# Kernel tuning notes

Measured on AMD Instinct MI355X. Metric: run time of the kernel, lower is better.

Reference implementation:

```python
import jax, jax.numpy as jnp
import numpy as np

EMBED_DIM = 768
N_HEADS = 12
HEAD_DIM = EMBED_DIM // N_HEADS
B, S = 8, 1024


def setup_inputs() -> dict:
    key = jax.random.key(0)
    ks = jax.random.split(key, 7)
    sc = 1.0 / np.sqrt(HEAD_DIM)
    return {
        "sequences": jax.random.normal(ks[0], (B, S, EMBED_DIM), dtype=jnp.float32),
        # per-head Linear weights stored [H, in, out] (torch Linear is x @ W.T + b;
        # with random init the layout convention is equivalent math)
        "Wq": jax.random.normal(ks[1], (N_HEADS, HEAD_DIM, HEAD_DIM), dtype=jnp.float32) * sc,
        "bq": jax.random.normal(ks[2], (N_HEADS, HEAD_DIM), dtype=jnp.float32) * 0.01,
        "Wk": jax.random.normal(ks[3], (N_HEADS, HEAD_DIM, HEAD_DIM), dtype=jnp.float32) * sc,
        "bk": jax.random.normal(ks[4], (N_HEADS, HEAD_DIM), dtype=jnp.float32) * 0.01,
        "Wv": jax.random.normal(ks[5], (N_HEADS, HEAD_DIM, HEAD_DIM), dtype=jnp.float32) * sc,
        "bv": jax.random.normal(ks[6], (N_HEADS, HEAD_DIM), dtype=jnp.float32) * 0.01,
    }


def reference(sequences, Wq, bq, Wk, bk, Wv, bv):
    b, s, d = sequences.shape
    h, hd = Wq.shape[0], Wq.shape[1]
    x = sequences.reshape(b, s, h, hd)              # split embed dim into heads
    q = jnp.einsum("bshd,hde->bshe", x, Wq) + bq    # per-head linear (block-diag GEMM)
    k = jnp.einsum("bshd,hde->bshe", x, Wk) + bk
    v = jnp.einsum("bshd,hde->bshe", x, Wv) + bv
    # NOTE: original module applies NO 1/sqrt(head_dim) scaling
    logits = jnp.einsum("bshe,bthe->bhst", q, k)    # [B,H,S,S]
    attn = jax.nn.softmax(logits, axis=-1)
    out = jnp.einsum("bhst,bthe->bshe", attn, v)    # [B,S,H,hd]
    return out.reshape(b, s, d)
```

## Files before the change

kernel.cpp:

```cpp
#include <hip/hip_runtime.h>
#include <stdint.h>

#define EMBED 768
#define NH 12
#define HD 64
#define Bsz 8
#define Ssz 1024
#define LOG2E 1.44269504088896f

typedef __attribute__((ext_vector_type(4))) float f32x4;
typedef __attribute__((ext_vector_type(8))) _Float16 f16x8;
typedef __attribute__((ext_vector_type(4))) _Float16 f16x4;

__launch_bounds__(256)
__global__ void qkv_proj(const float* __restrict__ x,
                         const float* __restrict__ Wq, const float* __restrict__ bq,
                         const float* __restrict__ Wk, const float* __restrict__ bk,
                         const float* __restrict__ Wv, const float* __restrict__ bv,
                         _Float16* __restrict__ Qb, _Float16* __restrict__ Kb,
                         _Float16* __restrict__ Vt)
{
    __shared__ _Float16 Xs[128 * 72];
    __shared__ _Float16 Wt[64 * 72];
    __shared__ _Float16 Ts[128 * 72];
    __shared__ float Bs[64];

    const int bt = blockIdx.x;
    const int st = bt & 7;
    const int h  = (bt >> 3) % NH;
    const int b  = bt / (8 * NH);
    const int sbase = st * 128;
    const int tid = threadIdx.x;
    const int lane = tid & 63, w = tid >> 6;
    const int l15 = lane & 15, quad = lane >> 4;

    for (int i = 0; i < 8; ++i) {
        int idx = tid + 256 * i;
        int row = idx >> 4;
        int c4  = (idx & 15) * 4;
        const float4 g = *(const float4*)&x[(size_t)(b * Ssz + sbase + row) * EMBED + h * HD + c4];
        f16x4 v; v[0] = (_Float16)g.x; v[1] = (_Float16)g.y; v[2] = (_Float16)g.z; v[3] = (_Float16)g.w;
        *(f16x4*)&Xs[row * 72 + c4] = v;
    }
    __syncthreads();

    f16x8 bx[2][2];
    const int nbg0 = w * 2;
#pragma unroll
    for (int nb = 0; nb < 2; ++nb)
#pragma unroll
        for (int kh = 0; kh < 2; ++kh)
            bx[nb][kh] = *(const f16x8*)&Xs[((nbg0 + nb) * 16 + l15) * 72 + kh * 32 + quad * 8];

    const float* Ws0[3] = {Wq, Wk, Wv};
    const float* bs0[3] = {bq, bk, bv};
    const size_t qkbase = (size_t)(b * NH + h) * Ssz + sbase;
    const f32x4 zero = {0.f, 0.f, 0.f, 0.f};

#pragma unroll
    for (int m = 0; m < 3; ++m) {
        {
            const float* W = Ws0[m] + (size_t)h * HD * HD;
            for (int i = 0; i < 4; ++i) {
                int idx = tid + 256 * i;
                int d = idx >> 4, e4 = (idx & 15) * 4;
                float4 g = *(const float4*)&W[d * 64 + e4];
                Wt[(e4 + 0) * 72 + d] = (_Float16)g.x;
                Wt[(e4 + 1) * 72 + d] = (_Float16)g.y;
                Wt[(e4 + 2) * 72 + d] = (_Float16)g.z;
                Wt[(e4 + 3) * 72 + d] = (_Float16)g.w;
            }
            if (tid < 64) Bs[tid] = bs0[m][h * HD + tid];
        }
        __syncthreads();

        f32x4 acc[2][4];
#pragma unroll
        for (int nb = 0; nb < 2; ++nb)
#pragma unroll
            for (int eb = 0; eb < 4; ++eb) acc[nb][eb] = zero;
#pragma unroll
        for (int eb = 0; eb < 4; ++eb)
#pragma unroll
            for (int kh = 0; kh < 2; ++kh) {
                f16x8 aw = *(const f16x8*)&Wt[(eb * 16 + l15) * 72 + kh * 32 + quad * 8];
#pragma unroll
                for (int nb = 0; nb < 2; ++nb)
                    acc[nb][eb] = __builtin_amdgcn_mfma_f32_16x16x32_f16(aw, bx[nb][kh], acc[nb][eb], 0, 0, 0);
            }

        if (m < 2) {
            const float sc = (m == 0) ? LOG2E : 1.0f;
#pragma unroll
            for (int nb = 0; nb < 2; ++nb)
#pragma unroll
                for (int eb = 0; eb < 4; ++eb) {
                    f32x4 bb = *(const f32x4*)&Bs[eb * 16 + quad * 4];
                    f16x4 v;
#pragma unroll
                    for (int r = 0; r < 4; ++r) v[r] = (_Float16)((acc[nb][eb][r] + bb[r]) * sc);
                    *(f16x4*)&Ts[((nbg0 + nb) * 16 + l15) * 72 + eb * 16 + quad * 4] = v;
                }
            __syncthreads();
            _Float16* outp = (m == 0) ? Qb : Kb;
            for (int i = 0; i < 4; ++i) {
                int idx = tid + 256 * i;
                int s = idx >> 3, e8 = (idx & 7) * 8;
                *(f16x8*)&outp[(qkbase + s) * HD + e8] = *(const f16x8*)&Ts[s * 72 + e8];
            }
            __syncthreads();
        } else {
            _Float16* Vs = Ts;
#pragma unroll
            for (int nb = 0; nb < 2; ++nb)
#pragma unroll
                for (int eb = 0; eb < 4; ++eb) {
                    f32x4 bb = *(const f32x4*)&Bs[eb * 16 + quad * 4];
#pragma unroll
                    for (int r = 0; r < 4; ++r)
                        Vs[(eb * 16 + quad * 4 + r) * 136 + (nbg0 + nb) * 16 + l15] =
                            (_Float16)(acc[nb][eb][r] + bb[r]);
                }
            __syncthreads();
            for (int i = 0; i < 4; ++i) {
                int idx = tid + 256 * i;
                int e = idx >> 4, s8 = (idx & 15) * 8;
                *(f16x8*)&Vt[((size_t)(b * NH + h) * 64 + e) * Ssz + sbase + s8] =
                    *(const f16x8*)&Vs[e * 136 + s8];
            }
        }
    }
}

__launch_bounds__(512)
__global__ void attn(const _Float16* __restrict__ Qb, const _Float16* __restrict__ Kb,
                     const _Float16* __restrict__ Vt, float* __restrict__ out)
{
    __shared__ _Float16 KV[2 * 9216];
    __shared__ _Float16 Pl[8 * 16 * 72];

    const int bt = blockIdx.x;
    const int qt = bt & 7;
    const int h  = (bt >> 3) % NH;
    const int b  = bt / (8 * NH);

    const int tid = threadIdx.x;
    const int lane = tid & 63, w = tid >> 6;
    const int l15 = lane & 15, quad = lane >> 4;

    const size_t bh = (size_t)(b * NH + h);
    const _Float16* Qg = Qb + bh * Ssz * HD;
    const _Float16* Kg = Kb + bh * Ssz * HD;
    const _Float16* Vg = Vt + bh * (size_t)HD * Ssz;

    const int qrow0 = qt * 128 + w * 16;
    f16x8 aq[2];
#pragma unroll
    for (int kh = 0; kh < 2; ++kh)
        aq[kh] = *(const f16x8*)&Qg[(qrow0 + l15) * HD + kh * 32 + quad * 8];

    const f32x4 zero = {0.f, 0.f, 0.f, 0.f};
    f32x4 o[4];
#pragma unroll
    for (int eb = 0; eb < 4; ++eb) o[eb] = zero;
    float m_run = -INFINITY, l_run = 0.f;

    const int srow = tid >> 3;
    const int scol = (tid & 7) * 8;

    f16x8 kr = *(const f16x8*)&Kg[srow * HD + scol];
    f16x8 vr = *(const f16x8*)&Vg[(size_t)srow * Ssz + scol];
    *(f16x8*)&KV[srow * 72 + scol] = kr;
    *(f16x8*)&KV[4608 + srow * 72 + scol] = vr;
    __syncthreads();

    _Float16* Pw = &Pl[(w * 16 + l15) * 72];

    for (int kt = 0; kt < 16; ++kt) {
        const int cur = kt & 1;
        if (kt < 15) {
            kr = *(const f16x8*)&Kg[((kt + 1) * 64 + srow) * HD + scol];
            vr = *(const f16x8*)&Vg[(size_t)srow * Ssz + (kt + 1) * 64 + scol];
        }
        const _Float16* Ksb = &KV[cur * 9216];
        const _Float16* Vsb = &KV[cur * 9216 + 4608];

        f32x4 st[4];
#pragma unroll
        for (int tb = 0; tb < 4; ++tb) {
            f32x4 acc = zero;
#pragma unroll
            for (int kh = 0; kh < 2; ++kh) {
                f16x8 ak = *(const f16x8*)&Ksb[(tb * 16 + l15) * 72 + kh * 32 + quad * 8];
                acc = __builtin_amdgcn_mfma_f32_16x16x32_f16(ak, aq[kh], acc, 0, 0, 0);
            }
            st[tb] = acc;
        }

        float mt = st[0][0];
#pragma unroll
        for (int tb = 0; tb < 4; ++tb)
#pragma unroll
            for (int r = 0; r < 4; ++r) mt = fmaxf(mt, st[tb][r]);
        mt = fmaxf(mt, __shfl_xor(mt, 16, 64));
        mt = fmaxf(mt, __shfl_xor(mt, 32, 64));
        float mn = fmaxf(m_run, mt);
        float al = exp2f(m_run - mn);
        float rs = 0.f;
        f16x4 pv[4];
#pragma unroll
        for (int tb = 0; tb < 4; ++tb) {
            float p0 = exp2f(st[tb][0] - mn);
            float p1 = exp2f(st[tb][1] - mn);
            float p2 = exp2f(st[tb][2] - mn);
            float p3 = exp2f(st[tb][3] - mn);
            rs += (p0 + p1) + (p2 + p3);
            pv[tb][0] = (_Float16)p0; pv[tb][1] = (_Float16)p1;
            pv[tb][2] = (_Float16)p2; pv[tb][3] = (_Float16)p3;
        }
        rs += __shfl_xor(rs, 16, 64);
        rs += __shfl_xor(rs, 32, 64);
        l_run = l_run * al + rs;
        m_run = mn;
#pragma unroll
        for (int eb = 0; eb < 4; ++eb) o[eb] *= al;

#pragma unroll
        for (int tb = 0; tb < 4; ++tb)
            *(f16x4*)&Pw[tb * 16 + quad * 4] = pv[tb];
        __asm__ __volatile__("s_waitcnt lgkmcnt(0)" ::: "memory");
        f16x8 bp[2];
#pragma unroll
        for (int kh = 0; kh < 2; ++kh)
            bp[kh] = *(const f16x8*)&Pw[kh * 32 + quad * 8];

#pragma unroll
        for (int kh = 0; kh < 2; ++kh)
#pragma unroll
            for (int eb = 0; eb < 4; ++eb) {
                f16x8 av = *(const f16x8*)&Vsb[(eb * 16 + l15) * 72 + kh * 32 + quad * 8];
                o[eb] = __builtin_amdgcn_mfma_f32_16x16x32_f16(av, bp[kh], o[eb], 0, 0, 0);
            }

        if (kt < 15) {
            const int nxt = cur ^ 1;
            *(f16x8*)&KV[nxt * 9216 + srow * 72 + scol] = kr;
            *(f16x8*)&KV[nxt * 9216 + 4608 + srow * 72 + scol] = vr;
        }
        __syncthreads();
    }

    const float inv = 1.f / l_run;
    const int q = qrow0 + l15;
    float* op = &out[(size_t)(b * Ssz + q) * EMBED + h * HD + quad * 4];
#pragma unroll
    for (int eb = 0; eb < 4; ++eb) {
        f32x4 r = o[eb] * inv;
        *(f32x4*)&op[eb * 16] = r;
    }
}

extern "C" void kernel_launch(void* const* d_in, const int* in_sizes, int n_in,
                              void* d_out, int out_size, void* d_ws, size_t ws_size,
                              hipStream_t stream) {
    const float* x  = (const float*)d_in[0];
    const float* Wq = (const float*)d_in[1];
    const float* bq = (const float*)d_in[2];
    const float* Wk = (const float*)d_in[3];
    const float* bk = (const float*)d_in[4];
    const float* Wv = (const float*)d_in[5];
    const float* bv = (const float*)d_in[6];

    _Float16* Qb = (_Float16*)d_ws;
    _Float16* Kb = Qb + (size_t)Bsz * NH * Ssz * HD;
    _Float16* Vt = Kb + (size_t)Bsz * NH * Ssz * HD;

    qkv_proj<<<dim3(Bsz * NH * 8), dim3(256), 0, stream>>>(x, Wq, bq, Wk, bk, Wv, bv, Qb, Kb, Vt);
    attn<<<dim3(Bsz * NH * 8), dim3(512), 0, stream>>>(Qb, Kb, Vt, (float*)d_out);
}
```

Measured before the change: 151.1 us.

## Swizzle attention LDS tiles, batch QKV weight loads, use fast exp2 and packed converts

The attention kernel replaces padded shared-memory rows (stride 72) with an XOR-swizzled stride-64 layout for the K, V and P tiles, aiming to avoid bank conflicts while using less LDS. It also reorders the block index so query tiles of the same head are spread apart, calls the hardware exp2 intrinsic directly, and converts to fp16 with packed round-toward-zero. The projection kernel loads all three weight matrices and biases up front behind a single barrier and reuses one staging buffer. The rtz conversion and raw exp2 may change rounding slightly, and the projection kernel uses more shared memory.

Result: faster. 136.7 us (median of 2 runs) (-9.6%).

```diff
diff --git a/kernel.cpp b/kernel.cpp
--- a/kernel.cpp
+++ b/kernel.cpp
@@ -11,6 +11,11 @@
 typedef __attribute__((ext_vector_type(4))) float f32x4;
 typedef __attribute__((ext_vector_type(8))) _Float16 f16x8;
 typedef __attribute__((ext_vector_type(4))) _Float16 f16x4;
+typedef __attribute__((ext_vector_type(2))) _Float16 f16x2;
+
+__device__ __forceinline__ int SW(int row, int col) {
+    return row * 64 + (col ^ ((row & 7) << 3));
+}
 
 __launch_bounds__(256)
 __global__ void qkv_proj(const float* __restrict__ x,
@@ -20,10 +25,9 @@
                          _Float16* __restrict__ Qb, _Float16* __restrict__ Kb,
                          _Float16* __restrict__ Vt)
 {
-    __shared__ _Float16 Xs[128 * 72];
-    __shared__ _Float16 Wt[64 * 72];
-    __shared__ _Float16 Ts[128 * 72];
-    __shared__ float Bs[64];
+    __shared__ _Float16 XT[128 * 72];
+    __shared__ _Float16 Wt[3 * 64 * 72];
+    __shared__ float Bs[192];
 
     const int bt = blockIdx.x;
     const int st = bt & 7;
@@ -40,40 +44,42 @@
         int c4  = (idx & 15) * 4;
         const float4 g = *(const float4*)&x[(size_t)(b * Ssz + sbase + row) * EMBED + h * HD + c4];
         f16x4 v; v[0] = (_Float16)g.x; v[1] = (_Float16)g.y; v[2] = (_Float16)g.z; v[3] = (_Float16)g.w;
-        *(f16x4*)&Xs[row * 72 + c4] = v;
-    }
-    __syncthreads();
-
-    f16x8 bx[2][2];
-    const int nbg0 = w * 2;
-#pragma unroll
-    for (int nb = 0; nb < 2; ++nb)
-#pragma unroll
-        for (int kh = 0; kh < 2; ++kh)
-            bx[nb][kh] = *(const f16x8*)&Xs[((nbg0 + nb) * 16 + l15) * 72 + kh * 32 + quad * 8];
-
-    const float* Ws0[3] = {Wq, Wk, Wv};
-    const float* bs0[3] = {bq, bk, bv};
-    const size_t qkbase = (size_t)(b * NH + h) * Ssz + sbase;
-    const f32x4 zero = {0.f, 0.f, 0.f, 0.f};
-
-#pragma unroll
-    for (int m = 0; m < 3; ++m) {
-        {
+        *(f16x4*)&XT[row * 72 + c4] = v;
+    }
+    {
+        const float* Ws0[3] = {Wq, Wk, Wv};
+        const float* bs0[3] = {bq, bk, bv};
+#pragma unroll
+        for (int m = 0; m < 3; ++m) {
             const float* W = Ws0[m] + (size_t)h * HD * HD;
             for (int i = 0; i < 4; ++i) {
                 int idx = tid + 256 * i;
                 int d = idx >> 4, e4 = (idx & 15) * 4;
                 float4 g = *(const float4*)&W[d * 64 + e4];
-                Wt[(e4 + 0) * 72 + d] = (_Float16)g.x;
-                Wt[(e4 + 1) * 72 + d] = (_Float16)g.y;
-                Wt[(e4 + 2) * 72 + d] = (_Float16)g.z;
-                Wt[(e4 + 3) * 72 + d] = (_Float16)g.w;
-            }
-            if (tid < 64) Bs[tid] = bs0[m][h * HD + tid];
-        }
-        __syncthreads();
-
+                Wt[m * 4608 + (e4 + 0) * 72 + d] = (_Float16)g.x;
+                Wt[m * 4608 + (e4 + 1) * 72 + d] = (_Float16)g.y;
+                Wt[m * 4608 + (e4 + 2) * 72 + d] = (_Float16)g.z;
+                Wt[m * 4608 + (e4 + 3) * 72 + d] = (_Float16)g.w;
+            }
+        }
+        if (tid < 192) Bs[tid] = bs0[tid >> 6][h * HD + (tid & 63)];
+    }
+    __syncthreads();
+
+    f16x8 bx[2][2];
+    const int nbg0 = w * 2;
+#pragma unroll
+    for (int nb = 0; nb < 2; ++nb)
+#pragma unroll
+        for (int kh = 0; kh < 2; ++kh)
+            bx[nb][kh] = *(const f16x8*)&XT[((nbg0 + nb) * 16 + l15) * 72 + kh * 32 + quad * 8];
+    __syncthreads();
+
+    const size_t qkbase = (size_t)(b * NH + h) * Ssz + sbase;
+    const f32x4 zero = {0.f, 0.f, 0.f, 0.f};
+
+#pragma unroll
+    for (int m = 0; m < 3; ++m) {
         f32x4 acc[2][4];
 #pragma unroll
         for (int nb = 0; nb < 2; ++nb)
@@ -83,7 +89,7 @@
         for (int eb = 0; eb < 4; ++eb)
 #pragma unroll
             for (int kh = 0; kh < 2; ++kh) {
-                f16x8 aw = *(const f16x8*)&Wt[(eb * 16 + l15) * 72 + kh * 32 + quad * 8];
+                f16x8 aw = *(const f16x8*)&Wt[m * 4608 + (eb * 16 + l15) * 72 + kh * 32 + quad * 8];
 #pragma unroll
                 for (int nb = 0; nb < 2; ++nb)
                     acc[nb][eb] = __builtin_amdgcn_mfma_f32_16x16x32_f16(aw, bx[nb][kh], acc[nb][eb], 0, 0, 0);
@@ -95,27 +101,27 @@
             for (int nb = 0; nb < 2; ++nb)
 #pragma unroll
                 for (int eb = 0; eb < 4; ++eb) {
-                    f32x4 bb = *(const f32x4*)&Bs[eb * 16 + quad * 4];
+                    f32x4 bb = *(const f32x4*)&Bs[m * 64 + eb * 16 + quad * 4];
                     f16x4 v;
 #pragma unroll
                     for (int r = 0; r < 4; ++r) v[r] = (_Float16)((acc[nb][eb][r] + bb[r]) * sc);
-                    *(f16x4*)&Ts[((nbg0 + nb) * 16 + l15) * 72 + eb * 16 + quad * 4] = v;
+                    *(f16x4*)&XT[((nbg0 + nb) * 16 + l15) * 72 + eb * 16 + quad * 4] = v;
                 }
             __syncthreads();
             _Float16* outp = (m == 0) ? Qb : Kb;
             for (int i = 0; i < 4; ++i) {
                 int idx = tid + 256 * i;
                 int s = idx >> 3, e8 = (idx & 7) * 8;
-                *(f16x8*)&outp[(qkbase + s) * HD + e8] = *(const f16x8*)&Ts[s * 72 + e8];
+                *(f16x8*)&outp[(qkbase + s) * HD + e8] = *(const f16x8*)&XT[s * 72 + e8];
             }
             __syncthreads();
         } else {
-            _Float16* Vs = Ts;
+            _Float16* Vs = XT;
 #pragma unroll
             for (int nb = 0; nb < 2; ++nb)
 #pragma unroll
                 for (int eb = 0; eb < 4; ++eb) {
-                    f32x4 bb = *(const f32x4*)&Bs[eb * 16 + quad * 4];
+                    f32x4 bb = *(const f32x4*)&Bs[128 + eb * 16 + quad * 4];
 #pragma unroll
                     for (int r = 0; r < 4; ++r)
                         Vs[(eb * 16 + quad * 4 + r) * 136 + (nbg0 + nb) * 16 + l15] =
@@ -136,13 +142,14 @@
 __global__ void attn(const _Float16* __restrict__ Qb, const _Float16* __restrict__ Kb,
                      const _Float16* __restrict__ Vt, float* __restrict__ out)
 {
-    __shared__ _Float16 KV[2 * 9216];
-    __shared__ _Float16 Pl[8 * 16 * 72];
+    __shared__ _Float16 KV[2 * 8192];
+    __shared__ _Float16 Pl[8 * 16 * 64];
 
     const int bt = blockIdx.x;
-    const int qt = bt & 7;
-    const int h  = (bt >> 3) % NH;
-    const int b  = bt / (8 * NH);
+    const int hh = bt % 96;
+    const int qt = bt / 96;
+    const int h  = hh % NH;
+    const int b  = hh / NH;
 
     const int tid = threadIdx.x;
     const int lane = tid & 63, w = tid >> 6;
@@ -167,14 +174,16 @@
 
     const int srow = tid >> 3;
     const int scol = (tid & 7) * 8;
+    const int swst = SW(srow, scol);
 
     f16x8 kr = *(const f16x8*)&Kg[srow * HD + scol];
     f16x8 vr = *(const f16x8*)&Vg[(size_t)srow * Ssz + scol];
-    *(f16x8*)&KV[srow * 72 + scol] = kr;
-    *(f16x8*)&KV[4608 + srow * 72 + scol] = vr;
+    *(f16x8*)&KV[swst] = kr;
+    *(f16x8*)&KV[4096 + swst] = vr;
     __syncthreads();
 
-    _Float16* Pw = &Pl[(w * 16 + l15) * 72];
+    _Float16* Pw = &Pl[w * 1024];
+    const int swq = (l15 & 7) << 3;
 
     for (int kt = 0; kt < 16; ++kt) {
         const int cur = kt & 1;
@@ -182,8 +191,8 @@
             kr = *(const f16x8*)&Kg[((kt + 1) * 64 + srow) * HD + scol];
             vr = *(const f16x8*)&Vg[(size_t)srow * Ssz + (kt + 1) * 64 + scol];
         }
-        const _Float16* Ksb = &KV[cur * 9216];
-        const _Float16* Vsb = &KV[cur * 9216 + 4608];
+        const _Float16* Ksb = &KV[cur * 8192];
+        const _Float16* Vsb = &KV[cur * 8192 + 4096];
 
         f32x4 st[4];
 #pragma unroll
@@ -191,7 +200,7 @@
             f32x4 acc = zero;
 #pragma unroll
             for (int kh = 0; kh < 2; ++kh) {
-                f16x8 ak = *(const f16x8*)&Ksb[(tb * 16 + l15) * 72 + kh * 32 + quad * 8];
+                f16x8 ak = *(const f16x8*)&Ksb[SW(tb * 16 + l15, kh * 32 + quad * 8)];
                 acc = __builtin_amdgcn_mfma_f32_16x16x32_f16(ak, aq[kh], acc, 0, 0, 0);
             }
             st[tb] = acc;
@@ -205,18 +214,19 @@
         mt = fmaxf(mt, __shfl_xor(mt, 16, 64));
         mt = fmaxf(mt, __shfl_xor(mt, 32, 64));
         float mn = fmaxf(m_run, mt);
-        float al = exp2f(m_run - mn);
+        float al = __builtin_amdgcn_exp2f(m_run - mn);
         float rs = 0.f;
         f16x4 pv[4];
 #pragma unroll
         for (int tb = 0; tb < 4; ++tb) {
-            float p0 = exp2f(st[tb][0] - mn);
-            float p1 = exp2f(st[tb][1] - mn);
-            float p2 = exp2f(st[tb][2] - mn);
-            float p3 = exp2f(st[tb][3] - mn);
+            float p0 = __builtin_amdgcn_exp2f(st[tb][0] - mn);
+            float p1 = __builtin_amdgcn_exp2f(st[tb][1] - mn);
+            float p2 = __builtin_amdgcn_exp2f(st[tb][2] - mn);
+            float p3 = __builtin_amdgcn_exp2f(st[tb][3] - mn);
             rs += (p0 + p1) + (p2 + p3);
-            pv[tb][0] = (_Float16)p0; pv[tb][1] = (_Float16)p1;
-            pv[tb][2] = (_Float16)p2; pv[tb][3] = (_Float16)p3;
+            f16x2 lo = __builtin_bit_cast(f16x2, __builtin_amdgcn_cvt_pkrtz(p0, p1));
+            f16x2 hi = __builtin_bit_cast(f16x2, __builtin_amdgcn_cvt_pkrtz(p2, p3));
+            pv[tb][0] = lo[0]; pv[tb][1] = lo[1]; pv[tb][2] = hi[0]; pv[tb][3] = hi[1];
         }
         rs += __shfl_xor(rs, 16, 64);
         rs += __shfl_xor(rs, 32, 64);
@@ -227,25 +237,25 @@
 
 #pragma unroll
         for (int tb = 0; tb < 4; ++tb)
-            *(f16x4*)&Pw[tb * 16 + quad * 4] = pv[tb];
+            *(f16x4*)&Pw[l15 * 64 + ((tb * 16 + quad * 4) ^ swq)] = pv[tb];
         __asm__ __volatile__("s_waitcnt lgkmcnt(0)" ::: "memory");
         f16x8 bp[2];
 #pragma unroll
         for (int kh = 0; kh < 2; ++kh)
-            bp[kh] = *(const f16x8*)&Pw[kh * 32 + quad * 8];
+            bp[kh] = *(const f16x8*)&Pw[l15 * 64 + ((kh * 32 + quad * 8) ^ swq)];
 
 #pragma unroll
         for (int kh = 0; kh < 2; ++kh)
 #pragma unroll
             for (int eb = 0; eb < 4; ++eb) {
-                f16x8 av = *(const f16x8*)&Vsb[(eb * 16 + l15) * 72 + kh * 32 + quad * 8];
+                f16x8 av = *(const f16x8*)&Vsb[SW(eb * 16 + l15, kh * 32 + quad * 8)];
                 o[eb] = __builtin_amdgcn_mfma_f32_16x16x32_f16(av, bp[kh], o[eb], 0, 0, 0);
             }
 
         if (kt < 15) {
             const int nxt = cur ^ 1;
-            *(f16x8*)&KV[nxt * 9216 + srow * 72 + scol] = kr;
-            *(f16x8*)&KV[nxt * 9216 + 4608 + srow * 72 + scol] = vr;
+            *(f16x8*)&KV[nxt * 8192 + swst] = kr;
+            *(f16x8*)&KV[nxt * 8192 + 4096 + swst] = vr;
         }
         __syncthreads();
     }
```
